# Performance work log

Hardware: AMD Instinct MI355X
Metric: run time of the kernel (lower is better)

Reference implementation:

```python
import jax, jax.numpy as jnp
import numpy as np

NUM_EXPERTS = 8
DIM = 1024
HIDDEN = 2048
N_TOKENS = 8192  # rows of x, includes padding beyond sum(num_tokens_per_expert)


def setup_inputs() -> dict:
    key = jax.random.key(0)
    k_x, k_w1, k_w2, k_w3 = jax.random.split(key, 4)
    x = jax.random.normal(k_x, (N_TOKENS, DIM), dtype=jnp.float32)
    # trunc_normal(std=0.02)-like init; w2 is zeros in torch init but we use
    w1 = jax.random.normal(k_w1, (NUM_EXPERTS, HIDDEN, DIM), dtype=jnp.float32) * 0.02
    w2 = jax.random.normal(k_w2, (NUM_EXPERTS, DIM, HIDDEN), dtype=jnp.float32) * 0.02
    w3 = jax.random.normal(k_w3, (NUM_EXPERTS, HIDDEN, DIM), dtype=jnp.float32) * 0.02
    # routed token counts per expert; sum <= N_TOKENS, remainder is padding
    num_tokens_per_expert = jnp.array([995, 1000, 980, 1010, 970, 1020, 990, 1005], dtype=jnp.int64)
    return {"x": x, "num_tokens_per_expert": num_tokens_per_expert,
            "w1": w1, "w2": w2, "w3": w3}


def reference(x, num_tokens_per_expert, w1, w2, w3):
    # Mirrors torch _run_experts_for_loop with act='silu'. The torch code calls
    # .tolist() on the counts (shapes are data-dependent), so we likewise treat
    # the per-expert counts as static host values.
    counts = np.asarray(num_tokens_per_expert).astype(np.int64)
    offsets = np.concatenate([np.zeros(1, np.int64), np.cumsum(counts)])
    total = int(offsets[-1])
    num_experts = w1.shape[0]
    out_splits = []
    for e in range(num_experts):
        xe = x[int(offsets[e]):int(offsets[e + 1])]            # [n_e, dim]
        gate = jax.nn.silu(xe @ w1[e].T)                       # [n_e, hidden]
        h = gate * (xe @ w3[e].T)                              # SwiGLU
        out_splits.append(h @ w2[e].T)                         # [n_e, dim]
    out = jnp.concatenate(out_splits, axis=0)
    num_padding = x.shape[0] - total
    if num_padding > 0:
        out = jnp.concatenate([out, jnp.zeros((num_padding, out.shape[-1]), out.dtype)], axis=0)
    return out
```

## Files before the change

### kernel.cpp

```cpp
#include <hip/hip_runtime.h>

#define NEXP 8
#define DIM  1024
#define HID  2048
#define NTOK 8192

#define BM 128
#define BN 128
#define BK 32

typedef short s16x8 __attribute__((ext_vector_type(8)));
typedef float f32x4 __attribute__((ext_vector_type(4)));
typedef unsigned short u16;

__device__ __forceinline__ u16 f2bf(float f) {
  unsigned int u = __builtin_bit_cast(unsigned int, f);
  u += 0x7FFFu + ((u >> 16) & 1u);
  return (u16)(u >> 16);
}

__device__ __forceinline__ s16x8 pk8(float4 a, float4 b) {
  union { unsigned u[4]; s16x8 v; } P;
  asm("v_cvt_pk_bf16_f32 %0, %1, %2" : "=v"(P.u[0]) : "v"(a.x), "v"(a.y));
  asm("v_cvt_pk_bf16_f32 %0, %1, %2" : "=v"(P.u[1]) : "v"(a.z), "v"(a.w));
  asm("v_cvt_pk_bf16_f32 %0, %1, %2" : "=v"(P.u[2]) : "v"(b.x), "v"(b.y));
  asm("v_cvt_pk_bf16_f32 %0, %1, %2" : "=v"(P.u[3]) : "v"(b.z), "v"(b.w));
  return P.v;
}

__device__ __forceinline__ void gload16(const u16* g, u16* l) {
  __builtin_amdgcn_global_load_lds((const __attribute__((address_space(1))) void*)g,
                                   (__attribute__((address_space(3))) void*)l, 16, 0, 0);
}

__device__ __forceinline__ bool find_tile(const int* __restrict__ cnts, int rt,
                                          int& e_out, int& row0, int& cnt_out, long long& off_out) {
  long long off = 0; int cum = 0;
  #pragma unroll
  for (int e = 0; e < NEXP; ++e) {
    int c = cnts[e];
    int nt = (c + BM - 1) / BM;
    if (rt < cum + nt) { e_out = e; row0 = (rt - cum) * BM; cnt_out = c; off_out = off; return true; }
    cum += nt; off += c;
  }
  return false;
}

#define XSTR 68
__global__ __launch_bounds__(512, 4) void gemm1_f32(
    const float* __restrict__ x, const int* __restrict__ cnts,
    const float* __restrict__ w1, const float* __restrict__ w3,
    u16* __restrict__ hbuf)
{
  int e, row0, cnt; long long off;
  if (!find_tile(cnts, blockIdx.y, e, row0, cnt, off)) return;
  const int ct = blockIdx.x;

  __shared__ __align__(16) float smem_f[4 * 64 * XSTR];
  u16* stage = (u16*)smem_f;

  const int t    = threadIdx.x;
  const int lane = t & 63;
  const int wid  = t >> 6;
  const int mat  = wid >> 2;
  const int sw   = wid & 3;
  const int wr = sw >> 1, wc = sw & 1;
  const int lr = lane & 15;
  const int lk = (((lane >> 4) ^ ((lr >> 1) & 3)) << 3);

  const int q    = lane >> 2;
  const int cf   = (lane & 3) ^ ((q >> 1) & 3);
  const int srow = wid * 16 + q;

  const float* xr  = x  + (size_t)(off + row0) * DIM;
  const float* w1t = w1 + ((size_t)e * HID + (size_t)ct * BN) * DIM;
  const float* w3t = w3 + ((size_t)e * HID + (size_t)ct * BN) * DIM;
  const size_t gbase = (size_t)srow * DIM + cf * 8;

  f32x4 acc[4][4];
  const f32x4 zf = {0.f, 0.f, 0.f, 0.f};
  #pragma unroll
  for (int i = 0; i < 4; ++i)
    #pragma unroll
    for (int j = 0; j < 4; ++j) acc[i][j] = zf;

  float4 Ra0, Ra1, Rb0, Rb1, Rc0, Rc1;
  auto LOADS = [&](int k0) {
    const size_t go = gbase + k0;
    Ra0 = *(const float4*)&xr [go]; Ra1 = *(const float4*)&xr [go + 4];
    Rb0 = *(const float4*)&w1t[go]; Rb1 = *(const float4*)&w1t[go + 4];
    Rc0 = *(const float4*)&w3t[go]; Rc1 = *(const float4*)&w3t[go + 4];
  };
  auto WRITE = [&](int b) {
    u16* base = stage + b * (3 * 4096) + wid * 512 + lane * 8;
    *(s16x8*)(base)        = pk8(Ra0, Ra1);
    *(s16x8*)(base + 4096) = pk8(Rb0, Rb1);
    *(s16x8*)(base + 8192) = pk8(Rc0, Rc1);
  };
  auto COMPUTE = [&](int b) {
    const u16* Asb = stage + b * (3 * 4096);
    const u16* Bsb = Asb + 4096 + mat * 4096;
    s16x8 af[4], bf[4];
    #pragma unroll
    for (int fm = 0; fm < 4; ++fm)
      af[fm] = *(const s16x8*)&Asb[(wr * 64 + fm * 16 + lr) * BK + lk];
    #pragma unroll
    for (int fn = 0; fn < 4; ++fn)
      bf[fn] = *(const s16x8*)&Bsb[(wc * 64 + fn * 16 + lr) * BK + lk];
    __builtin_amdgcn_s_setprio(1);
    #pragma unroll
    for (int fm = 0; fm < 4; ++fm)
      #pragma unroll
      for (int fn = 0; fn < 4; ++fn)
        acc[fm][fn] = __builtin_amdgcn_mfma_f32_16x16x32_bf16(af[fm], bf[fn], acc[fm][fn], 0, 0, 0);
    __builtin_amdgcn_s_setprio(0);
  };

  const int NT = DIM / BK;
  LOADS(0);
  WRITE(0);
  __syncthreads();
  int cur = 0;
  for (int kt = 0; kt < NT - 1; ++kt) {
    LOADS((kt + 1) * BK);
    COMPUTE(cur);
    WRITE(cur ^ 1);
    __syncthreads();
    cur ^= 1;
  }
  COMPUTE(cur);

  __syncthreads();
  if (mat) {
    float* up = smem_f + sw * (64 * XSTR);
    #pragma unroll
    for (int fm = 0; fm < 4; ++fm)
      #pragma unroll
      for (int fn = 0; fn < 4; ++fn)
        #pragma unroll
        for (int j = 0; j < 4; ++j)
          up[(fm * 16 + ((lane >> 4) << 2) + j) * XSTR + fn * 16 + lr] = acc[fm][fn][j];
  }
  __syncthreads();
  if (!mat) {
    const float* up = smem_f + sw * (64 * XSTR);
    #pragma unroll
    for (int fm = 0; fm < 4; ++fm)
      #pragma unroll
      for (int fn = 0; fn < 4; ++fn) {
        const int col = ct * BN + wc * 64 + fn * 16 + lr;
        #pragma unroll
        for (int j = 0; j < 4; ++j) {
          const int r = wr * 64 + fm * 16 + ((lane >> 4) << 2) + j;
          if (row0 + r < cnt) {
            const float gv = acc[fm][fn][j];
            const float uv = up[(fm * 16 + ((lane >> 4) << 2) + j) * XSTR + fn * 16 + lr];
            const float hv = (gv / (1.f + __expf(-gv))) * uv;
            hbuf[(size_t)(off + row0 + r) * HID + col] = f2bf(hv);
          }
        }
      }
  }
}

__global__ __launch_bounds__(256, 4) void gemm2_f32(
    const u16* __restrict__ hbuf, const int* __restrict__ cnts,
    const float* __restrict__ w2, float* __restrict__ out)
{
  int e, row0, cnt; long long off;
  if (!find_tile(cnts, blockIdx.y, e, row0, cnt, off)) return;
  const int ct = blockIdx.x;

  __shared__ __align__(16) u16 stage[2 * 2 * 4096];

  const int t    = threadIdx.x;
  const int lane = t & 63;
  const int wid  = t >> 6;
  const int wr = wid >> 1, wc = wid & 1;
  const int lr = lane & 15;
  const int lk = (((lane >> 4) ^ ((lr >> 1) & 3)) << 3);

  const int q  = lane >> 2;
  const int cf = (lane & 3) ^ ((q >> 1) & 3);

  const u16* ar    = hbuf + (size_t)(off + row0) * HID;
  const float* w2t = w2 + ((size_t)e * DIM + (size_t)ct * BN) * HID;

  f32x4 acc[4][4];
  const f32x4 zf = {0.f, 0.f, 0.f, 0.f};
  #pragma unroll
  for (int i = 0; i < 4; ++i)
    #pragma unroll
    for (int j = 0; j < 4; ++j) acc[i][j] = zf;

  float4 Rb[4];
  auto LOADS = [&](int k0, int b) {
    u16* Abase = stage + b * (2 * 4096);
    #pragma unroll
    for (int c = 0; c < 2; ++c) {
      const int chunk = wid * 2 + c;
      const int r = chunk * 16 + q;
      const size_t go = (size_t)r * HID + k0 + cf * 8;
      gload16(&ar[go], Abase + chunk * 512);
      Rb[2 * c]     = *(const float4*)&w2t[go];
      Rb[2 * c + 1] = *(const float4*)&w2t[go + 4];
    }
  };
  auto WRITEB = [&](int b) {
    u16* Bbase = stage + b * (2 * 4096) + 4096;
    *(s16x8*)(Bbase + (wid * 2 + 0) * 512 + lane * 8) = pk8(Rb[0], Rb[1]);
    *(s16x8*)(Bbase + (wid * 2 + 1) * 512 + lane * 8) = pk8(Rb[2], Rb[3]);
  };
  auto COMPUTE = [&](int b) {
    const u16* Asb = stage + b * (2 * 4096);
    const u16* Bsb = Asb + 4096;
    s16x8 af[4], bf[4];
    #pragma unroll
    for (int fm = 0; fm < 4; ++fm)
      af[fm] = *(const s16x8*)&Asb[(wr * 64 + fm * 16 + lr) * BK + lk];
    #pragma unroll
    for (int fn = 0; fn < 4; ++fn)
      bf[fn] = *(const s16x8*)&Bsb[(wc * 64 + fn * 16 + lr) * BK + lk];
    #pragma unroll
    for (int fm = 0; fm < 4; ++fm)
      #pragma unroll
      for (int fn = 0; fn < 4; ++fn)
        acc[fm][fn] = __builtin_amdgcn_mfma_f32_16x16x32_bf16(af[fm], bf[fn], acc[fm][fn], 0, 0, 0);
  };

  const int NT = HID / BK;
  LOADS(0, 0);
  WRITEB(0);
  __syncthreads();
  int cur = 0;
  for (int kt = 0; kt < NT - 1; ++kt) {
    LOADS((kt + 1) * BK, cur ^ 1);
    COMPUTE(cur);
    WRITEB(cur ^ 1);
    __syncthreads();
    cur ^= 1;
  }
  COMPUTE(cur);

  #pragma unroll
  for (int fm = 0; fm < 4; ++fm)
    #pragma unroll
    for (int fn = 0; fn < 4; ++fn) {
      const int col = ct * BN + wc * 64 + fn * 16 + lr;
      #pragma unroll
      for (int j = 0; j < 4; ++j) {
        const int r = wr * 64 + fm * 16 + ((lane >> 4) << 2) + j;
        if (row0 + r < cnt)
          out[(size_t)(off + row0 + r) * DIM + col] = acc[fm][fn][j];
      }
    }
}

__global__ void zero_pad_kernel(const int* __restrict__ cnts, float* __restrict__ out)
{
  int total = 0;
  #pragma unroll
  for (int e = 0; e < NEXP; ++e) total += cnts[e];
  const int row = blockIdx.x;
  if (row < total) return;
  float4* p = (float4*)(out + (size_t)row * DIM);
  p[threadIdx.x] = make_float4(0.f, 0.f, 0.f, 0.f);
}

extern "C" void kernel_launch(void* const* d_in, const int* in_sizes, int n_in,
                              void* d_out, int out_size, void* d_ws, size_t ws_size,
                              hipStream_t stream) {
  const float* x    = (const float*)d_in[0];
  const int*   cnts = (const int*)d_in[1];
  const float* w1   = (const float*)d_in[2];
  const float* w2   = (const float*)d_in[3];
  const float* w3   = (const float*)d_in[4];
  float*       out  = (float*)d_out;

  u16* hbuf = (u16*)d_ws;

  gemm1_f32<<<dim3(HID / BN, 72), dim3(512), 0, stream>>>(x, cnts, w1, w3, hbuf);
  gemm2_f32<<<dim3(DIM / BN, 72), dim3(256), 0, stream>>>(hbuf, cnts, w2, out);
  zero_pad_kernel<<<dim3(NTOK), dim3(256), 0, stream>>>(cnts, out);
}
```

Before: 233.6 us.

## Pre-convert x to bf16 and pipeline A tiles via async LDS DMA triple buffer

Adds a kernel that converts x to bf16 once, so gemm1 can stream activation tiles with global_load_lds DMA instead of loading fp32 and packing each tile in registers. Both GEMMs now keep a three-deep LDS ring for the A operand and a two-deep buffer for register-staged fp32 weights, with a lighter barrier that waits only on LDS counters. The goal is to hide global latency and cut per-tile conversion work, at the cost of an extra launch, extra memory traffic for the bf16 copy of x, and more LDS per block, which may reduce occupancy.

```diff
diff --git a/kernel.cpp b/kernel.cpp
--- a/kernel.cpp
+++ b/kernel.cpp
@@ -17,6 +17,10 @@
   unsigned int u = __builtin_bit_cast(unsigned int, f);
   u += 0x7FFFu + ((u >> 16) & 1u);
   return (u16)(u >> 16);
+}
+
+__device__ __forceinline__ ushort4 cvt4(float4 a) {
+  ushort4 r; r.x = f2bf(a.x); r.y = f2bf(a.y); r.z = f2bf(a.z); r.w = f2bf(a.w); return r;
 }
 
 __device__ __forceinline__ s16x8 pk8(float4 a, float4 b) {
@@ -33,6 +37,12 @@
                                    (__attribute__((address_space(3))) void*)l, 16, 0, 0);
 }
 
+__device__ __forceinline__ void BAR() {
+  asm volatile("s_waitcnt lgkmcnt(0)" ::: "memory");
+  __builtin_amdgcn_s_barrier();
+  asm volatile("" ::: "memory");
+}
+
 __device__ __forceinline__ bool find_tile(const int* __restrict__ cnts, int rt,
                                           int& e_out, int& row0, int& cnt_out, long long& off_out) {
   long long off = 0; int cum = 0;
@@ -46,9 +56,15 @@
   return false;
 }
 
+__global__ __launch_bounds__(256) void cvt_x(const float* __restrict__ in,
+                                             u16* __restrict__ out, int n4) {
+  const int i = blockIdx.x * 256 + threadIdx.x;
+  if (i < n4) ((ushort4*)out)[i] = cvt4(((const float4*)in)[i]);
+}
+
 #define XSTR 68
-__global__ __launch_bounds__(512, 4) void gemm1_f32(
-    const float* __restrict__ x, const int* __restrict__ cnts,
+__global__ __launch_bounds__(512, 4) void gemm1_hyb(
+    const u16* __restrict__ xb, const int* __restrict__ cnts,
     const float* __restrict__ w1, const float* __restrict__ w3,
     u16* __restrict__ hbuf)
 {
@@ -57,7 +73,7 @@
   const int ct = blockIdx.x;
 
   __shared__ __align__(16) float smem_f[4 * 64 * XSTR];
-  u16* stage = (u16*)smem_f;
+  u16* lds = (u16*)smem_f;
 
   const int t    = threadIdx.x;
   const int lane = t & 63;
@@ -72,10 +88,10 @@
   const int cf   = (lane & 3) ^ ((q >> 1) & 3);
   const int srow = wid * 16 + q;
 
-  const float* xr  = x  + (size_t)(off + row0) * DIM;
+  const u16*   xr  = xb + (size_t)(off + row0) * DIM;
   const float* w1t = w1 + ((size_t)e * HID + (size_t)ct * BN) * DIM;
   const float* w3t = w3 + ((size_t)e * HID + (size_t)ct * BN) * DIM;
-  const size_t gbase = (size_t)srow * DIM + cf * 8;
+  const size_t gaoff = (size_t)srow * DIM + cf * 8;
 
   f32x4 acc[4][4];
   const f32x4 zf = {0.f, 0.f, 0.f, 0.f};
@@ -84,22 +100,23 @@
     #pragma unroll
     for (int j = 0; j < 4; ++j) acc[i][j] = zf;
 
-  float4 Ra0, Ra1, Rb0, Rb1, Rc0, Rc1;
-  auto LOADS = [&](int k0) {
-    const size_t go = gbase + k0;
-    Ra0 = *(const float4*)&xr [go]; Ra1 = *(const float4*)&xr [go + 4];
-    Rb0 = *(const float4*)&w1t[go]; Rb1 = *(const float4*)&w1t[go + 4];
-    Rc0 = *(const float4*)&w3t[go]; Rc1 = *(const float4*)&w3t[go + 4];
-  };
-  auto WRITE = [&](int b) {
-    u16* base = stage + b * (3 * 4096) + wid * 512 + lane * 8;
-    *(s16x8*)(base)        = pk8(Ra0, Ra1);
-    *(s16x8*)(base + 4096) = pk8(Rb0, Rb1);
-    *(s16x8*)(base + 8192) = pk8(Rc0, Rc1);
-  };
-  auto COMPUTE = [&](int b) {
-    const u16* Asb = stage + b * (3 * 4096);
-    const u16* Bsb = Asb + 4096 + mat * 4096;
+  float4 S[4];
+  auto ADMA = [&](int k0, int ab) {
+    gload16(&xr[gaoff + k0], lds + ab * 4096 + wid * 512);
+  };
+  auto WLOAD = [&](int k0) {
+    const size_t go = gaoff + k0;
+    S[0] = *(const float4*)&w1t[go]; S[1] = *(const float4*)&w1t[go + 4];
+    S[2] = *(const float4*)&w3t[go]; S[3] = *(const float4*)&w3t[go + 4];
+  };
+  auto WRITE_W = [&](int wb) {
+    u16* base = lds + 12288 + wb * 8192 + wid * 512 + lane * 8;
+    *(s16x8*)(base)        = pk8(S[0], S[1]);
+    *(s16x8*)(base + 4096) = pk8(S[2], S[3]);
+  };
+  auto COMPUTE = [&](int ab, int wb) {
+    const u16* Asb = lds + ab * 4096;
+    const u16* Bsb = lds + 12288 + wb * 8192 + mat * 4096;
     s16x8 af[4], bf[4];
     #pragma unroll
     for (int fm = 0; fm < 4; ++fm)
@@ -117,18 +134,21 @@
   };
 
   const int NT = DIM / BK;
-  LOADS(0);
-  WRITE(0);
-  __syncthreads();
-  int cur = 0;
-  for (int kt = 0; kt < NT - 1; ++kt) {
-    LOADS((kt + 1) * BK);
-    COMPUTE(cur);
-    WRITE(cur ^ 1);
-    __syncthreads();
-    cur ^= 1;
-  }
-  COMPUTE(cur);
+  ADMA(0, 0);
+  ADMA(BK, 1);
+  WLOAD(0);
+  WRITE_W(0);
+  WLOAD(BK);
+  BAR();
+  for (int kt = 0; kt < NT; ++kt) {
+    if (kt + 2 < NT) ADMA((kt + 2) * BK, (kt + 2) % 3);
+    COMPUTE(kt % 3, kt & 1);
+    if (kt + 1 < NT) {
+      WRITE_W((kt + 1) & 1);
+      if (kt + 2 < NT) WLOAD((kt + 2) * BK);
+    }
+    BAR();
+  }
 
   __syncthreads();
   if (mat) {
@@ -163,7 +183,7 @@
   }
 }
 
-__global__ __launch_bounds__(256, 4) void gemm2_f32(
+__global__ __launch_bounds__(256, 4) void gemm2_hyb(
     const u16* __restrict__ hbuf, const int* __restrict__ cnts,
     const float* __restrict__ w2, float* __restrict__ out)
 {
@@ -171,7 +191,7 @@
   if (!find_tile(cnts, blockIdx.y, e, row0, cnt, off)) return;
   const int ct = blockIdx.x;
 
-  __shared__ __align__(16) u16 stage[2 * 2 * 4096];
+  __shared__ __align__(16) u16 lds[20480];
 
   const int t    = threadIdx.x;
   const int lane = t & 63;
@@ -183,8 +203,10 @@
   const int q  = lane >> 2;
   const int cf = (lane & 3) ^ ((q >> 1) & 3);
 
-  const u16* ar    = hbuf + (size_t)(off + row0) * HID;
+  const u16*   ar  = hbuf + (size_t)(off + row0) * HID;
   const float* w2t = w2 + ((size_t)e * DIM + (size_t)ct * BN) * HID;
+  const size_t g0 = (size_t)(wid * 32 + q) * HID + cf * 8;
+  const size_t g1 = (size_t)(wid * 32 + 16 + q) * HID + cf * 8;
 
   f32x4 acc[4][4];
   const f32x4 zf = {0.f, 0.f, 0.f, 0.f};
@@ -193,27 +215,24 @@
     #pragma unroll
     for (int j = 0; j < 4; ++j) acc[i][j] = zf;
 
-  float4 Rb[4];
-  auto LOADS = [&](int k0, int b) {
-    u16* Abase = stage + b * (2 * 4096);
-    #pragma unroll
-    for (int c = 0; c < 2; ++c) {
-      const int chunk = wid * 2 + c;
-      const int r = chunk * 16 + q;
-      const size_t go = (size_t)r * HID + k0 + cf * 8;
-      gload16(&ar[go], Abase + chunk * 512);
-      Rb[2 * c]     = *(const float4*)&w2t[go];
-      Rb[2 * c + 1] = *(const float4*)&w2t[go + 4];
-    }
-  };
-  auto WRITEB = [&](int b) {
-    u16* Bbase = stage + b * (2 * 4096) + 4096;
-    *(s16x8*)(Bbase + (wid * 2 + 0) * 512 + lane * 8) = pk8(Rb[0], Rb[1]);
-    *(s16x8*)(Bbase + (wid * 2 + 1) * 512 + lane * 8) = pk8(Rb[2], Rb[3]);
-  };
-  auto COMPUTE = [&](int b) {
-    const u16* Asb = stage + b * (2 * 4096);
-    const u16* Bsb = Asb + 4096;
+  float4 S[4];
+  auto ADMA = [&](int k0, int ab) {
+    u16* base = lds + ab * 4096;
+    gload16(&ar[g0 + k0], base + (wid * 2 + 0) * 512);
+    gload16(&ar[g1 + k0], base + (wid * 2 + 1) * 512);
+  };
+  auto WLOAD = [&](int k0) {
+    S[0] = *(const float4*)&w2t[g0 + k0]; S[1] = *(const float4*)&w2t[g0 + k0 + 4];
+    S[2] = *(const float4*)&w2t[g1 + k0]; S[3] = *(const float4*)&w2t[g1 + k0 + 4];
+  };
+  auto WRITE_W = [&](int wb) {
+    u16* base = lds + 12288 + wb * 4096;
+    *(s16x8*)(base + (wid * 2 + 0) * 512 + lane * 8) = pk8(S[0], S[1]);
+    *(s16x8*)(base + (wid * 2 + 1) * 512 + lane * 8) = pk8(S[2], S[3]);
+  };
+  auto COMPUTE = [&](int ab, int wb) {
+    const u16* Asb = lds + ab * 4096;
+    const u16* Bsb = lds + 12288 + wb * 4096;
     s16x8 af[4], bf[4];
     #pragma unroll
     for (int fm = 0; fm < 4; ++fm)
@@ -229,18 +248,21 @@
   };
 
   const int NT = HID / BK;
-  LOADS(0, 0);
-  WRITEB(0);
-  __syncthreads();
-  int cur = 0;
-  for (int kt = 0; kt < NT - 1; ++kt) {
-    LOADS((kt + 1) * BK, cur ^ 1);
-    COMPUTE(cur);
-    WRITEB(cur ^ 1);
-    __syncthreads();
-    cur ^= 1;
-  }
-  COMPUTE(cur);
+  ADMA(0, 0);
+  ADMA(BK, 1);
+  WLOAD(0);
+  WRITE_W(0);
+  WLOAD(BK);
+  BAR();
+  for (int kt = 0; kt < NT; ++kt) {
+    if (kt + 2 < NT) ADMA((kt + 2) * BK, (kt + 2) % 3);
+    COMPUTE(kt % 3, kt & 1);
+    if (kt + 1 < NT) {
+      WRITE_W((kt + 1) & 1);
+      if (kt + 2 < NT) WLOAD((kt + 2) * BK);
+    }
+    BAR();
+  }
 
   #pragma unroll
   for (int fm = 0; fm < 4; ++fm)
@@ -278,8 +300,11 @@
   float*       out  = (float*)d_out;
 
   u16* hbuf = (u16*)d_ws;
-
-  gemm1_f32<<<dim3(HID / BN, 72), dim3(512), 0, stream>>>(x, cnts, w1, w3, hbuf);
-  gemm2_f32<<<dim3(DIM / BN, 72), dim3(256), 0, stream>>>(hbuf, cnts, w2, out);
+  u16* xb   = hbuf + (size_t)NTOK * HID;
+
+  const int X4 = NTOK * DIM / 4;
+  cvt_x<<<dim3(X4 / 256), dim3(256), 0, stream>>>(x, xb, X4);
+  gemm1_hyb<<<dim3(HID / BN, 72), dim3(512), 0, stream>>>(xb, cnts, w1, w3, hbuf);
+  gemm2_hyb<<<dim3(DIM / BN, 72), dim3(256), 0, stream>>>(hbuf, cnts, w2, out);
   zero_pad_kernel<<<dim3(NTOK), dim3(256), 0, stream>>>(cnts, out);
 }
```

Result: faster. 202.6 us (-13.3%).
